# Kernel optimization log

Hardware: AMD Instinct MI355X
Metric: run time of the kernel (lower is better)

The kernel has to match this reference:

```python
import jax, jax.numpy as jnp
import numpy as np

IGNORE = -100
RANK_ALPHA = 1.0
CLAMP_MIN = 1e-5
BS, SEQ, VOCAB = 4, 512, 32000


def setup_inputs() -> dict:
    key = jax.random.key(0)
    k1, k2, k3, k4, k5 = jax.random.split(key, 5)
    logits = jax.random.normal(k1, (BS, SEQ, VOCAB), dtype=jnp.float32)
    target_user = jax.random.randint(k2, (BS, SEQ), 0, VOCAB, dtype=jnp.int32)
    target_res = jax.random.randint(k3, (BS, SEQ), 0, VOCAB, dtype=jnp.int32)
    belief_end = jax.random.randint(k4, (BS,), 0, SEQ, dtype=jnp.int32)
    res_end = jax.random.randint(k5, (BS,), 0, SEQ, dtype=jnp.int32)
    return {"logits": logits, "target_user": target_user, "target_res": target_res,
            "belief_end": belief_end, "res_end": res_end}


def reference(logits, target_user, target_res, belief_end, res_end):
    bs, seq, vocab = logits.shape
    lprobs = jax.nn.log_softmax(logits, axis=-1)  # (bs, seq, vocab)

    # ---- MLE / NLL term (reduction='none', then sum; ignore_index masked) ----
    valid = target_res != IGNORE
    tr = jnp.where(valid, target_res, 0)
    nll = -jnp.take_along_axis(lprobs, tr[..., None], axis=-1)[..., 0]  # (bs, seq)
    mle_loss = jnp.sum(jnp.where(valid, nll, 0.0))

    # ---- Positive (user-overlap) term ----
    # ntarget = target_user + 1, ignore -> 0. scatter_ into (vocab+1) one-hot
    # collapses duplicates => per-batch set membership over the vocab.
    ntarget = jnp.where(target_user == IGNORE, 0, target_user + 1)  # (bs, seq)
    user_set = jnp.zeros((bs, vocab + 1), lprobs.dtype)
    user_set = user_set.at[jnp.arange(bs)[:, None], ntarget].set(1.0)
    user_set = user_set[:, 1:]  # drop padding slot (scatter of zeros at index 0)

    probs = jnp.clip(jnp.exp(lprobs), CLAMP_MIN)  # torch.clamp(lprobs.exp(), min=1e-5)
    cl = jnp.einsum('bsv,bv->bs', probs, user_set)  # sum of clamped probs over user-token set

    # end_ = max(seq, res_end[i]) >= seq, so row mask is simply i >= belief_end[b]
    row_mask = jnp.arange(seq)[None, :] >= belief_end[:, None]  # (bs, seq)
    cl = jnp.where(row_mask, cl, 0.0)

    pos = cl > 0
    custom_loss = jnp.sum(jnp.where(pos, -jnp.log(jnp.where(pos, cl, 1.0)), 0.0))

    loss = mle_loss + RANK_ALPHA * custom_loss
    weight = jnp.sum(valid).astype(lprobs.dtype)
    return loss / weight
```

## Files before the change

kernel.cpp:

```cpp
#include <hip/hip_runtime.h>
#include <math.h>

#define IGNORE_IDX (-100)
#define CLAMP_MIN 1e-5f

constexpr int BS = 4, SEQ = 512, VOCAB = 32000;
constexpr int WORDS = VOCAB / 32;
constexpr int NF4   = VOCAB / 4;
constexpr int NT    = 256;
constexpr int ACC_OFF_BYTES = 256;

__global__ void build_mask_kernel(const int* __restrict__ target_user,
                                  unsigned* __restrict__ mask) {
    int i = blockIdx.x * blockDim.x + threadIdx.x;
    if (i >= BS * SEQ) return;
    int b = i / SEQ;
    int v = target_user[i];
    if (v != IGNORE_IDX) atomicOr(&mask[b * WORDS + (v >> 5)], 1u << (v & 31));
}

__global__ __launch_bounds__(256)
void UserRepeatCrossEntropyCriterion_65060164599829_kernel(
    const float* __restrict__ logits,
    const int* __restrict__ target_res,
    const int* __restrict__ belief_end,
    const unsigned* __restrict__ mask,
    float* __restrict__ acc)
{
    const int row = blockIdx.x;
    const int b   = row >> 9;
    const int s   = row & (SEQ - 1);
    const float* __restrict__ x = logits + (size_t)row * VOCAB;
    const float4* __restrict__ x4 = (const float4*)x;
    const int tid = threadIdx.x;

    __shared__ int   toks[SEQ];
    __shared__ float stash[SEQ];
    __shared__ int   cnt;
    __shared__ float red[4];
    __shared__ float lse_sh;

    if (tid == 0) cnt = 0;
    __syncthreads();

    for (int w = tid; w < WORDS; w += NT) {
        unsigned bits = mask[b * WORDS + w];
        while (bits) {
            int bit = __ffs(bits) - 1;
            bits &= bits - 1;
            toks[atomicAdd(&cnt, 1)] = (w << 5) + bit;
        }
    }
    __syncthreads();
    const int n = cnt;

    for (int j = tid; j < n; j += NT) stash[j] = x[toks[j]];

    const int tr = target_res[row];
    float tgt_logit = 0.f;
    if (tid == 0 && tr != IGNORE_IDX) tgt_logit = x[tr];

    float s0 = 0.f, s1 = 0.f, s2 = 0.f, s3 = 0.f;
    int i = tid;
    for (int q = 0; q < 7; ++q, i += 4 * NT) {
        float4 a = x4[i];
        float4 c = x4[i + NT];
        float4 d = x4[i + 2 * NT];
        float4 e = x4[i + 3 * NT];
        s0 += __expf(a.x) + __expf(a.y) + __expf(a.z) + __expf(a.w);
        s1 += __expf(c.x) + __expf(c.y) + __expf(c.z) + __expf(c.w);
        s2 += __expf(d.x) + __expf(d.y) + __expf(d.z) + __expf(d.w);
        s3 += __expf(e.x) + __expf(e.y) + __expf(e.z) + __expf(e.w);
    }
    for (; i < NF4; i += NT) {
        float4 a = x4[i];
        s0 += __expf(a.x) + __expf(a.y) + __expf(a.z) + __expf(a.w);
    }
    float sum = (s0 + s1) + (s2 + s3);

    for (int off = 32; off >= 1; off >>= 1) sum += __shfl_down(sum, off);
    const int wave = tid >> 6;
    if ((tid & 63) == 0) red[wave] = sum;
    __syncthreads();
    if (tid == 0) lse_sh = __logf(red[0] + red[1] + red[2] + red[3]);
    __syncthreads();
    const float lse = lse_sh;

    float cl = 0.f;
    for (int j = tid; j < n; j += NT)
        cl += fmaxf(__expf(stash[j] - lse), CLAMP_MIN);
    for (int off = 32; off >= 1; off >>= 1) cl += __shfl_down(cl, off);
    if ((tid & 63) == 0) red[wave] = cl;
    __syncthreads();

    if (tid == 0) {
        float cl_total = red[0] + red[1] + red[2] + red[3];
        float contrib = 0.f, wgt = 0.f;
        if (tr != IGNORE_IDX) { contrib += lse - tgt_logit; wgt = 1.f; }
        if (s >= belief_end[b] && cl_total > 0.f) contrib += -__logf(cl_total);
        atomicAdd(&acc[0], contrib);
        atomicAdd(&acc[1], wgt);
    }
}

__global__ void finalize_kernel(const float* __restrict__ acc,
                                float* __restrict__ out) {
    out[0] = acc[0] / acc[1];
}

extern "C" void kernel_launch(void* const* d_in, const int* in_sizes, int n_in,
                              void* d_out, int out_size, void* d_ws, size_t ws_size,
                              hipStream_t stream) {
    const float* logits      = (const float*)d_in[0];
    const int*   target_user = (const int*)d_in[1];
    const int*   target_res  = (const int*)d_in[2];
    const int*   belief_end  = (const int*)d_in[3];
    float* out = (float*)d_out;

    float*    acc  = (float*)d_ws;
    unsigned* mask = (unsigned*)((char*)d_ws + ACC_OFF_BYTES);

    hipMemsetAsync(d_ws, 0, ACC_OFF_BYTES + (size_t)BS * WORDS * sizeof(unsigned), stream);

    build_mask_kernel<<<(BS * SEQ + 255) / 256, 256, 0, stream>>>(target_user, mask);

    UserRepeatCrossEntropyCriterion_65060164599829_kernel
        <<<BS * SEQ, NT, 0, stream>>>(logits, target_res, belief_end, mask, acc);

    finalize_kernel<<<1, 1, 0, stream>>>(acc, out);
}
```

Baseline: 382.4 us.

## Split row sum-exp across 8 slice blocks and gather user-set logits separately

The per-row sum of exponentials is split across 8 blocks per row, each covering 1000 float4s and atomically adding its partial sum into a per-row workspace value. A second kernel then computes the log-sum-exp, gathers the user-set logits straight from the bitmask, and skips that gather for rows before belief_end. This raises the number of blocks eightfold to expose more memory parallelism on the 262 MB stream, but adds an extra kernel launch, per-row atomics and a second pass of scattered reads over the logits.

```diff
diff --git a/kernel.cpp b/kernel.cpp
--- a/kernel.cpp
+++ b/kernel.cpp
@@ -3,12 +3,18 @@
 
 #define IGNORE_IDX (-100)
 #define CLAMP_MIN 1e-5f
+#define NEG_BIG (-1e30f)
 
 constexpr int BS = 4, SEQ = 512, VOCAB = 32000;
 constexpr int WORDS = VOCAB / 32;
 constexpr int NF4   = VOCAB / 4;
 constexpr int NT    = 256;
-constexpr int ACC_OFF_BYTES = 256;
+constexpr int SLICES = 8;
+constexpr int F4_PER_SLICE = NF4 / SLICES;
+
+constexpr int ROWSUM_OFF = 256;
+constexpr int MASK_OFF   = ROWSUM_OFF + BS * SEQ * 4;
+constexpr int WS_ZERO    = MASK_OFF + BS * WORDS * 4;
 
 __global__ void build_mask_kernel(const int* __restrict__ target_user,
                                   unsigned* __restrict__ mask) {
@@ -22,82 +28,76 @@
 __global__ __launch_bounds__(256)
 void UserRepeatCrossEntropyCriterion_65060164599829_kernel(
     const float* __restrict__ logits,
-    const int* __restrict__ target_res,
-    const int* __restrict__ belief_end,
-    const unsigned* __restrict__ mask,
-    float* __restrict__ acc)
+    float* __restrict__ rowsum)
+{
+    const int row   = blockIdx.x >> 3;
+    const int slice = blockIdx.x & (SLICES - 1);
+    const float4* __restrict__ x4 =
+        (const float4*)(logits + (size_t)row * VOCAB) + slice * F4_PER_SLICE;
+    const int tid = threadIdx.x;
+
+    float4 a = x4[tid];
+    float4 c = x4[tid + NT];
+    float4 d = x4[tid + 2 * NT];
+    float4 e = (tid + 3 * NT < F4_PER_SLICE)
+                   ? x4[tid + 3 * NT]
+                   : make_float4(NEG_BIG, NEG_BIG, NEG_BIG, NEG_BIG);
+
+    float s0 = __expf(a.x) + __expf(a.y) + __expf(a.z) + __expf(a.w);
+    float s1 = __expf(c.x) + __expf(c.y) + __expf(c.z) + __expf(c.w);
+    float s2 = __expf(d.x) + __expf(d.y) + __expf(d.z) + __expf(d.w);
+    float s3 = __expf(e.x) + __expf(e.y) + __expf(e.z) + __expf(e.w);
+    float sum = (s0 + s1) + (s2 + s3);
+
+    for (int off = 32; off >= 1; off >>= 1) sum += __shfl_down(sum, off);
+    __shared__ float red[4];
+    const int wave = tid >> 6;
+    if ((tid & 63) == 0) red[wave] = sum;
+    __syncthreads();
+    if (tid == 0)
+        atomicAdd(&rowsum[row], (red[0] + red[1]) + (red[2] + red[3]));
+}
+
+__global__ __launch_bounds__(256)
+void finish_kernel(const float* __restrict__ logits,
+                   const int* __restrict__ target_res,
+                   const int* __restrict__ belief_end,
+                   const unsigned* __restrict__ mask,
+                   const float* __restrict__ rowsum,
+                   float* __restrict__ acc)
 {
     const int row = blockIdx.x;
     const int b   = row >> 9;
     const int s   = row & (SEQ - 1);
     const float* __restrict__ x = logits + (size_t)row * VOCAB;
-    const float4* __restrict__ x4 = (const float4*)x;
     const int tid = threadIdx.x;
 
-    __shared__ int   toks[SEQ];
-    __shared__ float stash[SEQ];
-    __shared__ int   cnt;
-    __shared__ float red[4];
-    __shared__ float lse_sh;
+    const float lse = __logf(rowsum[row]);
+    const bool need_cl = (s >= belief_end[b]);
 
-    if (tid == 0) cnt = 0;
-    __syncthreads();
-
-    for (int w = tid; w < WORDS; w += NT) {
-        unsigned bits = mask[b * WORDS + w];
-        while (bits) {
-            int bit = __ffs(bits) - 1;
-            bits &= bits - 1;
-            toks[atomicAdd(&cnt, 1)] = (w << 5) + bit;
+    float cl = 0.f;
+    if (need_cl) {
+        for (int w = tid; w < WORDS; w += NT) {
+            unsigned bits = mask[b * WORDS + w];
+            while (bits) {
+                int bit = __ffs(bits) - 1;
+                bits &= bits - 1;
+                cl += fmaxf(__expf(x[(w << 5) + bit] - lse), CLAMP_MIN);
+            }
         }
     }
-    __syncthreads();
-    const int n = cnt;
-
-    for (int j = tid; j < n; j += NT) stash[j] = x[toks[j]];
-
-    const int tr = target_res[row];
-    float tgt_logit = 0.f;
-    if (tid == 0 && tr != IGNORE_IDX) tgt_logit = x[tr];
-
-    float s0 = 0.f, s1 = 0.f, s2 = 0.f, s3 = 0.f;
-    int i = tid;
-    for (int q = 0; q < 7; ++q, i += 4 * NT) {
-        float4 a = x4[i];
-        float4 c = x4[i + NT];
-        float4 d = x4[i + 2 * NT];
-        float4 e = x4[i + 3 * NT];
-        s0 += __expf(a.x) + __expf(a.y) + __expf(a.z) + __expf(a.w);
-        s1 += __expf(c.x) + __expf(c.y) + __expf(c.z) + __expf(c.w);
-        s2 += __expf(d.x) + __expf(d.y) + __expf(d.z) + __expf(d.w);
-        s3 += __expf(e.x) + __expf(e.y) + __expf(e.z) + __expf(e.w);
-    }
-    for (; i < NF4; i += NT) {
-        float4 a = x4[i];
-        s0 += __expf(a.x) + __expf(a.y) + __expf(a.z) + __expf(a.w);
-    }
-    float sum = (s0 + s1) + (s2 + s3);
-
-    for (int off = 32; off >= 1; off >>= 1) sum += __shfl_down(sum, off);
+    for (int off = 32; off >= 1; off >>= 1) cl += __shfl_down(cl, off);
+    __shared__ float red[4];
     const int wave = tid >> 6;
-    if ((tid & 63) == 0) red[wave] = sum;
-    __syncthreads();
-    if (tid == 0) lse_sh = __logf(red[0] + red[1] + red[2] + red[3]);
-    __syncthreads();
-    const float lse = lse_sh;
-
-    float cl = 0.f;
-    for (int j = tid; j < n; j += NT)
-        cl += fmaxf(__expf(stash[j] - lse), CLAMP_MIN);
-    for (int off = 32; off >= 1; off >>= 1) cl += __shfl_down(cl, off);
     if ((tid & 63) == 0) red[wave] = cl;
     __syncthreads();
 
     if (tid == 0) {
-        float cl_total = red[0] + red[1] + red[2] + red[3];
+        float cl_total = (red[0] + red[1]) + (red[2] + red[3]);
         float contrib = 0.f, wgt = 0.f;
-        if (tr != IGNORE_IDX) { contrib += lse - tgt_logit; wgt = 1.f; }
-        if (s >= belief_end[b] && cl_total > 0.f) contrib += -__logf(cl_total);
+        int tr = target_res[row];
+        if (tr != IGNORE_IDX) { contrib += lse - x[tr]; wgt = 1.f; }
+        if (need_cl && cl_total > 0.f) contrib += -__logf(cl_total);
         atomicAdd(&acc[0], contrib);
         atomicAdd(&acc[1], wgt);
     }
@@ -117,15 +117,19 @@
     const int*   belief_end  = (const int*)d_in[3];
     float* out = (float*)d_out;
 
-    float*    acc  = (float*)d_ws;
-    unsigned* mask = (unsigned*)((char*)d_ws + ACC_OFF_BYTES);
+    float*    acc    = (float*)d_ws;
+    float*    rowsum = (float*)((char*)d_ws + ROWSUM_OFF);
+    unsigned* mask   = (unsigned*)((char*)d_ws + MASK_OFF);
 
-    hipMemsetAsync(d_ws, 0, ACC_OFF_BYTES + (size_t)BS * WORDS * sizeof(unsigned), stream);
+    hipMemsetAsync(d_ws, 0, WS_ZERO, stream);
 
     build_mask_kernel<<<(BS * SEQ + 255) / 256, 256, 0, stream>>>(target_user, mask);
 
     UserRepeatCrossEntropyCriterion_65060164599829_kernel
-        <<<BS * SEQ, NT, 0, stream>>>(logits, target_res, belief_end, mask, acc);
+        <<<BS * SEQ * SLICES, NT, 0, stream>>>(logits, rowsum);
+
+    finish_kernel<<<BS * SEQ, NT, 0, stream>>>(logits, target_res, belief_end,
+                                               mask, rowsum, acc);
 
     finalize_kernel<<<1, 1, 0, stream>>>(acc, out);
 }
```

After: 416.2 us. 8.8% more time.

## Fuse user-set mask build into main kernel and gather set logits from registers

Applied to the files above, without the earlier changes.

Drops the separate mask-building kernel and its global memset. Each block now builds its own per-batch bitmask in shared memory with LDS atomics, and only for rows at or past belief_end. The row is streamed through an 8-deep float4 register prefetch pipeline, and logits in the user set are picked up from the values already in registers rather than through scattered global gathers. This removes one launch and the random gather reads, at the cost of redundant per-block mask construction and extra branching in the hot loop.

```diff
diff --git a/kernel.cpp b/kernel.cpp
--- a/kernel.cpp
+++ b/kernel.cpp
@@ -3,78 +3,91 @@
 
 #define IGNORE_IDX (-100)
 #define CLAMP_MIN 1e-5f
+#define NEG_BIG (-1e30f)
 
 constexpr int BS = 4, SEQ = 512, VOCAB = 32000;
 constexpr int WORDS = VOCAB / 32;
 constexpr int NF4   = VOCAB / 4;
 constexpr int NT    = 256;
-constexpr int ACC_OFF_BYTES = 256;
-
-__global__ void build_mask_kernel(const int* __restrict__ target_user,
-                                  unsigned* __restrict__ mask) {
-    int i = blockIdx.x * blockDim.x + threadIdx.x;
-    if (i >= BS * SEQ) return;
-    int b = i / SEQ;
-    int v = target_user[i];
-    if (v != IGNORE_IDX) atomicOr(&mask[b * WORDS + (v >> 5)], 1u << (v & 31));
-}
 
 __global__ __launch_bounds__(256)
 void UserRepeatCrossEntropyCriterion_65060164599829_kernel(
     const float* __restrict__ logits,
+    const int* __restrict__ target_user,
     const int* __restrict__ target_res,
     const int* __restrict__ belief_end,
-    const unsigned* __restrict__ mask,
     float* __restrict__ acc)
 {
     const int row = blockIdx.x;
     const int b   = row >> 9;
     const int s   = row & (SEQ - 1);
-    const float* __restrict__ x = logits + (size_t)row * VOCAB;
+    const float* __restrict__ x  = logits + (size_t)row * VOCAB;
     const float4* __restrict__ x4 = (const float4*)x;
     const int tid = threadIdx.x;
 
-    __shared__ int   toks[SEQ];
-    __shared__ float stash[SEQ];
-    __shared__ int   cnt;
-    __shared__ float red[4];
-    __shared__ float lse_sh;
+    float4 v[8];
+    #pragma unroll
+    for (int j = 0; j < 8; j++) v[j] = x4[tid + j * NT];
 
+    __shared__ unsigned smask[WORDS];
+    __shared__ float    stash[SEQ];
+    __shared__ int      cnt;
+    __shared__ float    red[4];
+    __shared__ float    lse_sh;
+
+    const bool need_cl = (s >= belief_end[b]);
+
+    for (int w = tid; w < WORDS; w += NT) smask[w] = 0u;
     if (tid == 0) cnt = 0;
     __syncthreads();
-
-    for (int w = tid; w < WORDS; w += NT) {
-        unsigned bits = mask[b * WORDS + w];
-        while (bits) {
-            int bit = __ffs(bits) - 1;
-            bits &= bits - 1;
-            toks[atomicAdd(&cnt, 1)] = (w << 5) + bit;
+    if (need_cl) {
+        #pragma unroll
+        for (int k = 0; k < SEQ / NT; k++) {
+            int tv = target_user[b * SEQ + k * NT + tid];
+            if (tv != IGNORE_IDX) atomicOr(&smask[tv >> 5], 1u << (tv & 31));
         }
     }
     __syncthreads();
-    const int n = cnt;
-
-    for (int j = tid; j < n; j += NT) stash[j] = x[toks[j]];
 
     const int tr = target_res[row];
     float tgt_logit = 0.f;
     if (tid == 0 && tr != IGNORE_IDX) tgt_logit = x[tr];
 
     float s0 = 0.f, s1 = 0.f, s2 = 0.f, s3 = 0.f;
-    int i = tid;
-    for (int q = 0; q < 7; ++q, i += 4 * NT) {
-        float4 a = x4[i];
-        float4 c = x4[i + NT];
-        float4 d = x4[i + 2 * NT];
-        float4 e = x4[i + 3 * NT];
-        s0 += __expf(a.x) + __expf(a.y) + __expf(a.z) + __expf(a.w);
-        s1 += __expf(c.x) + __expf(c.y) + __expf(c.z) + __expf(c.w);
-        s2 += __expf(d.x) + __expf(d.y) + __expf(d.z) + __expf(d.w);
-        s3 += __expf(e.x) + __expf(e.y) + __expf(e.z) + __expf(e.w);
-    }
-    for (; i < NF4; i += NT) {
-        float4 a = x4[i];
-        s0 += __expf(a.x) + __expf(a.y) + __expf(a.z) + __expf(a.w);
+    #pragma unroll
+    for (int g = 0; g < 4; g++) {
+        float4 nv[8];
+        if (g < 3) {
+            #pragma unroll
+            for (int j = 0; j < 8; j++) {
+                const int i = tid + ((g + 1) * 8 + j) * NT;
+                if (g < 2 || j < 7) {
+                    nv[j] = x4[i];
+                } else {
+                    nv[j] = (i < NF4) ? x4[i]
+                                      : make_float4(NEG_BIG, NEG_BIG, NEG_BIG, NEG_BIG);
+                }
+            }
+        }
+        #pragma unroll
+        for (int j = 0; j < 8; j++) {
+            const float4 a = v[j];
+            const int    i = tid + (g * 8 + j) * NT;
+            float e0 = __expf(a.x), e1 = __expf(a.y),
+                  e2 = __expf(a.z), e3 = __expf(a.w);
+            s0 += e0; s1 += e1; s2 += e2; s3 += e3;
+            if (need_cl && i < NF4) {
+                unsigned bits = (smask[i >> 3] >> ((i & 7) * 4)) & 0xFu;
+                if (bits) {
+                    if (bits & 1u) stash[atomicAdd(&cnt, 1)] = a.x;
+                    if (bits & 2u) stash[atomicAdd(&cnt, 1)] = a.y;
+                    if (bits & 4u) stash[atomicAdd(&cnt, 1)] = a.z;
+                    if (bits & 8u) stash[atomicAdd(&cnt, 1)] = a.w;
+                }
+            }
+        }
+        #pragma unroll
+        for (int j = 0; j < 8; j++) v[j] = nv[j];
     }
     float sum = (s0 + s1) + (s2 + s3);
 
@@ -82,22 +95,25 @@
     const int wave = tid >> 6;
     if ((tid & 63) == 0) red[wave] = sum;
     __syncthreads();
-    if (tid == 0) lse_sh = __logf(red[0] + red[1] + red[2] + red[3]);
+    if (tid == 0) lse_sh = __logf((red[0] + red[1]) + (red[2] + red[3]));
     __syncthreads();
     const float lse = lse_sh;
 
     float cl = 0.f;
-    for (int j = tid; j < n; j += NT)
-        cl += fmaxf(__expf(stash[j] - lse), CLAMP_MIN);
+    if (need_cl) {
+        const int n = cnt;
+        for (int j = tid; j < n; j += NT)
+            cl += fmaxf(__expf(stash[j] - lse), CLAMP_MIN);
+    }
     for (int off = 32; off >= 1; off >>= 1) cl += __shfl_down(cl, off);
     if ((tid & 63) == 0) red[wave] = cl;
     __syncthreads();
 
     if (tid == 0) {
-        float cl_total = red[0] + red[1] + red[2] + red[3];
+        float cl_total = (red[0] + red[1]) + (red[2] + red[3]);
         float contrib = 0.f, wgt = 0.f;
         if (tr != IGNORE_IDX) { contrib += lse - tgt_logit; wgt = 1.f; }
-        if (s >= belief_end[b] && cl_total > 0.f) contrib += -__logf(cl_total);
+        if (need_cl && cl_total > 0.f) contrib += -__logf(cl_total);
         atomicAdd(&acc[0], contrib);
         atomicAdd(&acc[1], wgt);
     }
@@ -116,16 +132,13 @@
     const int*   target_res  = (const int*)d_in[2];
     const int*   belief_end  = (const int*)d_in[3];
     float* out = (float*)d_out;
+    float* acc = (float*)d_ws;
 
-    float*    acc  = (float*)d_ws;
-    unsigned* mask = (unsigned*)((char*)d_ws + ACC_OFF_BYTES);
-
-    hipMemsetAsync(d_ws, 0, ACC_OFF_BYTES + (size_t)BS * WORDS * sizeof(unsigned), stream);
-
-    build_mask_kernel<<<(BS * SEQ + 255) / 256, 256, 0, stream>>>(target_user, mask);
+    hipMemsetAsync(d_ws, 0, 64, stream);
 
     UserRepeatCrossEntropyCriterion_65060164599829_kernel
-        <<<BS * SEQ, NT, 0, stream>>>(logits, target_res, belief_end, mask, acc);
+        <<<BS * SEQ, NT, 0, stream>>>(logits, target_user, target_res,
+                                      belief_end, acc);
 
     finalize_kernel<<<1, 1, 0, stream>>>(acc, out);
 }
```

Result: faster. 369.9 us (-3.3%).
